# Performance work log

Measured on AMD Instinct MI355X. Metric: run time of the kernel, lower is better.

Reference implementation:

```python
import jax, jax.numpy as jnp
import numpy as np

N_NODES = 100000
N_EDGES = 1600000
IN_CH = 128
HID = 128
N_REL = 8


def setup_inputs() -> dict:
    key = jax.random.key(0)
    k_x, k_src, k_dst, k_et, k_w, k_root, k_b = jax.random.split(key, 7)
    x = jax.random.normal(k_x, (N_NODES, IN_CH), dtype=jnp.float32)
    src = jax.random.randint(k_src, (N_EDGES,), 0, N_NODES)
    dst = jax.random.randint(k_dst, (N_EDGES,), 0, N_NODES)
    edge_index = jnp.stack([src, dst], axis=0)  # [2, E]
    edge_type = jax.random.randint(k_et, (N_EDGES,), 0, N_REL)
    # RGCNConv parameters: per-relation weight, root (self-loop) weight, bias
    scale = 1.0 / np.sqrt(IN_CH)
    W = jax.random.normal(k_w, (N_REL, IN_CH, HID), dtype=jnp.float32) * scale
    root = jax.random.normal(k_root, (IN_CH, HID), dtype=jnp.float32) * scale
    bias = jnp.zeros((HID,), dtype=jnp.float32)
    return {"x": x, "edge_index": edge_index, "edge_type": edge_type,
            "W": W, "root": root, "bias": bias}


def reference(x, edge_index, edge_type, W, root, bias):
    # RGCNConv (mean aggregation per relation) + ReLU. Dropout is identity (eval mode).
    # Aggregate-then-transform: mathematically identical to PyG's
    # transform-then-aggregate since the relation transform is linear,
    # but far cheaper (R matmuls over N nodes instead of E edges).
    N = x.shape[0]
    n_rel = W.shape[0]
    src, dst = edge_index[0], edge_index[1]
    x_src = x[src]  # [E, C] gathered neighbor features
    out = x @ root + bias  # root / self-loop term
    for r in range(n_rel):
        mask = (edge_type == r)
        xm = jnp.where(mask[:, None], x_src, 0.0)  # zero out other relations
        agg = jax.ops.segment_sum(xm, dst, num_segments=N)  # [N, C]
        cnt = jax.ops.segment_sum(mask.astype(x.dtype), dst, num_segments=N)
        mean_agg = agg / jnp.maximum(cnt, 1.0)[:, None]
        out = out + mean_agg @ W[r]
    return jax.nn.relu(out)
```

## Files before the change

### kernel.cpp

```cpp
#include <hip/hip_runtime.h>

#define NREL 8
#define CH   128
#define YW   1152
#define YWD  (YW / 2)
#define NCB2 18

#define SCAN_ITEMS   16
#define SCAN_THREADS 256
#define SCAN_CHUNK   (SCAN_ITEMS * SCAN_THREADS)
#define SCAN_SHIFT   12

typedef short  short8v __attribute__((ext_vector_type(8)));
typedef float  f32x4   __attribute__((ext_vector_type(4)));

__device__ __forceinline__ unsigned short f2bf(float f) {
    union { float f; unsigned u; } v; v.f = f;
    return (unsigned short)((v.u + 0x7FFFu + ((v.u >> 16) & 1u)) >> 16);
}
__device__ __forceinline__ float lof(unsigned u) {
    union { unsigned u; float f; } v; v.u = u << 16; return v.f;
}
__device__ __forceinline__ float hif(unsigned u) {
    union { unsigned u; float f; } v; v.u = u & 0xFFFF0000u; return v.f;
}
__device__ __forceinline__ void gload_lds16(const void* g, void* l) {
    __builtin_amdgcn_global_load_lds(
        (const __attribute__((address_space(1))) unsigned int*)g,
        (__attribute__((address_space(3))) unsigned int*)l, 16, 0, 0);
}

__global__ __launch_bounds__(256) void bt2_kernel(
    const float* __restrict__ W, const float* __restrict__ root,
    unsigned short* __restrict__ Bt2)
{
    int idx = blockIdx.x * blockDim.x + threadIdx.x;
    if (idx >= YW * CH) return;
    int rc = idx >> 7, k = idx & 127;
    int r = rc >> 7, c = rc & 127;
    float v = (r < NREL) ? W[(size_t)(r * CH + k) * CH + c]
                         : root[(size_t)k * CH + c];
    Bt2[idx] = f2bf(v);
}

__global__ __launch_bounds__(256) void hist_rank_kernel(
    const int* __restrict__ dst, const int* __restrict__ et,
    int* __restrict__ hist, int* __restrict__ rank, int E)
{
    int e = blockIdx.x * blockDim.x + threadIdx.x;
    if (e < E) rank[e] = atomicAdd(&hist[dst[e] * NREL + et[e]], 1);
}

__global__ __launch_bounds__(SCAN_THREADS) void scan1_kernel(
    const int* __restrict__ hist, int* __restrict__ pad_offs,
    int* __restrict__ partials, int S)
{
    __shared__ int lds[SCAN_THREADS];
    int t = threadIdx.x;
    int base = blockIdx.x * SCAN_CHUNK + t * SCAN_ITEMS;
    int v[SCAN_ITEMS];
    int s = 0;
#pragma unroll
    for (int j = 0; j < SCAN_ITEMS; j++) {
        int idx = base + j;
        int h = (idx < S) ? hist[idx] : 0;
        v[j] = s; s += h;
    }
    int run = s;
    lds[t] = run; __syncthreads();
    for (int off = 1; off < SCAN_THREADS; off <<= 1) {
        int y = (t >= off) ? lds[t - off] : 0;
        __syncthreads();
        run += y; lds[t] = run; __syncthreads();
    }
    int tb = run - s;
    if (t == SCAN_THREADS - 1) partials[blockIdx.x] = run;
#pragma unroll
    for (int j = 0; j < SCAN_ITEMS; j++) {
        int idx = base + j;
        if (idx < S) pad_offs[idx] = tb + v[j];
    }
}

__global__ __launch_bounds__(SCAN_THREADS) void scan2_kernel(
    int* __restrict__ partials, int NB)
{
    __shared__ int lds[SCAN_THREADS];
    int t = threadIdx.x;
    int s = (t < NB) ? partials[t] : 0;
    int run = s;
    lds[t] = run; __syncthreads();
    for (int off = 1; off < SCAN_THREADS; off <<= 1) {
        int y = (t >= off) ? lds[t - off] : 0;
        __syncthreads();
        run += y; lds[t] = run; __syncthreads();
    }
    if (t < NB) partials[t] = run - s;
}

__global__ __launch_bounds__(256) void finalize_kernel(
    int* __restrict__ pad_offs, const int* __restrict__ partials, int S, int E)
{
    int i = blockIdx.x * blockDim.x + threadIdx.x;
    if (i < S)       pad_offs[i] += partials[i >> SCAN_SHIFT];
    else if (i == S) pad_offs[i] = E;
}

__global__ __launch_bounds__(512, 6) void ygemm_fill_kernel(
    const float* __restrict__ x,
    const unsigned short* __restrict__ Bt2,
    unsigned short* __restrict__ y,
    int N,
    const int* __restrict__ src, const int* __restrict__ dst,
    const int* __restrict__ et, const int* __restrict__ rank,
    const int* __restrict__ pad_offs,
    int* __restrict__ perm, int E, int epb)
{
    __shared__ __align__(16) unsigned short As[128 * 128];
    __shared__ __align__(16) unsigned short Bs[64 * 128];

    int tid  = threadIdx.x;
    int lane = tid & 63;
    int wid  = tid >> 6;
    int wm   = wid >> 2;
    int wn   = wid & 3;
    int r15  = lane & 15;
    int kg   = lane >> 4;
    int n0   = blockIdx.x * 128;

    int eb   = blockIdx.x * epb;
    int elim = eb + epb; if (elim > E) elim = E;
    int p0 = -1, p1 = -1, p2 = -1, p3 = -1;
    int v0 = 0, v1 = 0, v2 = 0, v3 = 0;
    {
        int e0 = eb + tid;
        int e1 = e0 + 512, e2 = e1 + 512, e3 = e2 + 512;
        if (e0 < elim) { int t0 = et[e0]; v0 = (src[e0] << 3) | t0;
                         p0 = pad_offs[dst[e0] * NREL + t0] + rank[e0]; }
        if (e1 < elim) { int t1 = et[e1]; v1 = (src[e1] << 3) | t1;
                         p1 = pad_offs[dst[e1] * NREL + t1] + rank[e1]; }
        if (e2 < elim) { int t2 = et[e2]; v2 = (src[e2] << 3) | t2;
                         p2 = pad_offs[dst[e2] * NREL + t2] + rank[e2]; }
        if (e3 < elim) { int t3 = et[e3]; v3 = (src[e3] << 3) | t3;
                         p3 = pad_offs[dst[e3] * NREL + t3] + rank[e3]; }
    }

    {
        int row = tid >> 2;
        int kq  = tid & 3;
        int gn  = n0 + row; if (gn >= N) gn = N - 1;
        const float* xp = x + (size_t)gn * CH + kq * 32;
#pragma unroll
        for (int s8 = 0; s8 < 4; ++s8) {
            float4 f0 = *(const float4*)(xp + s8 * 8);
            float4 f1 = *(const float4*)(xp + s8 * 8 + 4);
            uint4 v;
            v.x = f2bf(f0.x) | ((unsigned)f2bf(f0.y) << 16);
            v.y = f2bf(f0.z) | ((unsigned)f2bf(f0.w) << 16);
            v.z = f2bf(f1.x) | ((unsigned)f2bf(f1.y) << 16);
            v.w = f2bf(f1.z) | ((unsigned)f2bf(f1.w) << 16);
            int slot = kq * 4 + s8;
            int phys = slot ^ (row & 15);
            *(uint4*)&As[row * 128 + phys * 8] = v;
        }
    }

    for (int cb = 0; cb < NCB2; ++cb) {
#pragma unroll
        for (int i = 0; i < 2; ++i) {
            int chunk = wid * 2 + i;
            int col   = chunk * 4 + (lane >> 4);
            int slot  = (lane & 15) ^ (col & 15);
            const char* srcp = (const char*)(Bt2 + (size_t)(cb * 64 + col) * CH + slot * 8);
            gload_lds16(srcp, &Bs[chunk * 512]);
        }
        __syncthreads();

        if      (cb == 1) { if (p0 >= 0) perm[p0] = v0; }
        else if (cb == 2) { if (p1 >= 0) perm[p1] = v1; }
        else if (cb == 3) { if (p2 >= 0) perm[p2] = v2; }
        else if (cb == 4) { if (p3 >= 0) perm[p3] = v3; }

        f32x4 acc[4];
#pragma unroll
        for (int i = 0; i < 4; i++) acc[i] = f32x4{0.f, 0.f, 0.f, 0.f};

#pragma unroll
        for (int ks = 0; ks < 4; ++ks) {
            short8v a[4], b;
#pragma unroll
            for (int mr = 0; mr < 4; ++mr) {
                int row  = wm * 64 + mr * 16 + r15;
                int phys = (ks * 4 + kg) ^ (row & 15);
                a[mr] = *(const short8v*)&As[row * 128 + phys * 8];
            }
            {
                int col  = wn * 16 + r15;
                int phys = (ks * 4 + kg) ^ (col & 15);
                b = *(const short8v*)&Bs[col * 128 + phys * 8];
            }
#pragma unroll
            for (int mr = 0; mr < 4; ++mr)
                acc[mr] = __builtin_amdgcn_mfma_f32_16x16x32_bf16(
                    a[mr], b, acc[mr], 0, 0, 0);
        }

#pragma unroll
        for (int mr = 0; mr < 4; ++mr) {
#pragma unroll
            for (int reg = 0; reg < 4; ++reg) {
                int gr = n0 + wm * 64 + mr * 16 + kg * 4 + reg;
                if (gr >= N) continue;
                int gc = cb * 64 + wn * 16 + r15;
                y[(size_t)gr * YW + gc] = f2bf(acc[mr][reg]);
            }
        }
        __syncthreads();
    }
}

__global__ __launch_bounds__(256) void gather_kernel(
    const unsigned short* __restrict__ y,
    const int* __restrict__ perm,
    const int* __restrict__ pad_offs,
    const int* __restrict__ hist,
    const float* __restrict__ bias,
    float* __restrict__ out, int N)
{
    int wid  = threadIdx.x >> 6;
    int lane = threadIdx.x & 63;
    int n    = blockIdx.x * 4 + wid;
    if (n >= N) return;

    int beg = pad_offs[n * NREL];
    int end = pad_offs[n * NREL + NREL];

    int4 h0 = *(const int4*)(hist + (size_t)n * NREL);
    int4 h1 = *(const int4*)(hist + (size_t)n * NREL + 4);
    float iw0 = 1.0f / (float)max(h0.x, 1);
    float iw1 = 1.0f / (float)max(h0.y, 1);
    float iw2 = 1.0f / (float)max(h0.z, 1);
    float iw3 = 1.0f / (float)max(h0.w, 1);
    float iw4 = 1.0f / (float)max(h1.x, 1);
    float iw5 = 1.0f / (float)max(h1.y, 1);
    float iw6 = 1.0f / (float)max(h1.z, 1);
    float iw7 = 1.0f / (float)max(h1.w, 1);

    const unsigned* y32 = (const unsigned*)y;
    float a0 = 0.f, a1 = 0.f;

    for (int blk = beg; blk < end; blk += 64) {
        int m = end - blk; if (m > 64) m = 64;
        int   rv = 0;
        float wv = 0.f;
        if (lane < m) {
            int pv  = perm[blk + lane];
            int rel = pv & 7;
            rv = pv + (pv >> 3);
            float wa = (rel & 1) ? iw1 : iw0;
            float wb = (rel & 1) ? iw3 : iw2;
            float wc = (rel & 1) ? iw5 : iw4;
            float wd = (rel & 1) ? iw7 : iw6;
            float we_ = (rel & 2) ? wb : wa;
            float wf  = (rel & 2) ? wd : wc;
            wv = (rel & 4) ? wf : we_;
        }

        int j = 0;
#define EDGE_LOAD(K) \
            int   p##K = __shfl(rv, j + K);                     \
            float w##K = __shfl(wv, j + K);                     \
            unsigned u##K = y32[(size_t)p##K * 64 + lane];
#define EDGE_ACC(K) \
            a0 += w##K * lof(u##K); a1 += w##K * hif(u##K);

        for (; j + 16 <= m; j += 16) {
            EDGE_LOAD(0) EDGE_LOAD(1) EDGE_LOAD(2)  EDGE_LOAD(3)
            EDGE_LOAD(4) EDGE_LOAD(5) EDGE_LOAD(6)  EDGE_LOAD(7)
            EDGE_LOAD(8) EDGE_LOAD(9) EDGE_LOAD(10) EDGE_LOAD(11)
            EDGE_LOAD(12) EDGE_LOAD(13) EDGE_LOAD(14) EDGE_LOAD(15)
            EDGE_ACC(0)  EDGE_ACC(1)  EDGE_ACC(2)  EDGE_ACC(3)
            EDGE_ACC(4)  EDGE_ACC(5)  EDGE_ACC(6)  EDGE_ACC(7)
            EDGE_ACC(8)  EDGE_ACC(9)  EDGE_ACC(10) EDGE_ACC(11)
            EDGE_ACC(12) EDGE_ACC(13) EDGE_ACC(14) EDGE_ACC(15)
        }
        if (j + 8 <= m) {
            EDGE_LOAD(0) EDGE_LOAD(1) EDGE_LOAD(2) EDGE_LOAD(3)
            EDGE_LOAD(4) EDGE_LOAD(5) EDGE_LOAD(6) EDGE_LOAD(7)
            EDGE_ACC(0) EDGE_ACC(1) EDGE_ACC(2) EDGE_ACC(3)
            EDGE_ACC(4) EDGE_ACC(5) EDGE_ACC(6) EDGE_ACC(7)
            j += 8;
        }
        if (j + 4 <= m) {
            EDGE_LOAD(0) EDGE_LOAD(1) EDGE_LOAD(2) EDGE_LOAD(3)
            EDGE_ACC(0) EDGE_ACC(1) EDGE_ACC(2) EDGE_ACC(3)
            j += 4;
        }
        for (; j < m; ++j) {
            EDGE_LOAD(0)
            EDGE_ACC(0)
        }
#undef EDGE_LOAD
#undef EDGE_ACC
    }

    unsigned ur = y32[(size_t)n * YWD + (NREL * CH / 2) + lane];
    float o0 = a0 + lof(ur) + bias[lane * 2];
    float o1 = a1 + hif(ur) + bias[lane * 2 + 1];
    float2 ov;
    ov.x = fmaxf(o0, 0.f);
    ov.y = fmaxf(o1, 0.f);
    *(float2*)(out + (size_t)n * CH + lane * 2) = ov;
}

extern "C" void kernel_launch(void* const* d_in, const int* in_sizes, int n_in,
                              void* d_out, int out_size, void* d_ws, size_t ws_size,
                              hipStream_t stream)
{
    const float* x    = (const float*)d_in[0];
    const int*   ei   = (const int*)d_in[1];
    const int*   et   = (const int*)d_in[2];
    const float* W    = (const float*)d_in[3];
    const float* root = (const float*)d_in[4];
    const float* bias = (const float*)d_in[5];
    float*       out  = (float*)d_out;

    int N = in_sizes[0] / CH;
    int E = in_sizes[2];
    const int* src = ei;
    const int* dst = ei + E;

    int S  = N * NREL;
    int NB = (S + SCAN_CHUNK - 1) / SCAN_CHUNK;

    unsigned short* y   = (unsigned short*)d_ws;
    unsigned short* Bt2 = y + (size_t)N * YW;
    int* hist     = (int*)(Bt2 + (size_t)YW * CH);
    int* pad_offs = hist + S;
    int* partials = pad_offs + S + 1;
    int* perm     = partials + 256;
    int* rank     = perm + E;

    hipMemsetAsync(hist, 0, (size_t)S * sizeof(int), stream);

    int egrid = (E + 255) / 256;
    int G     = (N + 127) / 128;
    int epb   = ((E + G - 1) / G + 2047) & ~2047;

    bt2_kernel<<<(YW * CH + 255) / 256, 256, 0, stream>>>(W, root, Bt2);
    hist_rank_kernel<<<egrid, 256, 0, stream>>>(dst, et, hist, rank, E);
    scan1_kernel<<<NB, SCAN_THREADS, 0, stream>>>(hist, pad_offs, partials, S);
    scan2_kernel<<<1, SCAN_THREADS, 0, stream>>>(partials, NB);
    finalize_kernel<<<(S + 256) / 256, 256, 0, stream>>>(pad_offs, partials, S, E);
    ygemm_fill_kernel<<<G, 512, 0, stream>>>(x, Bt2, y, N,
                                             src, dst, et, rank, pad_offs,
                                             perm, E, epb);
    gather_kernel<<<(N + 3) / 4, 256, 0, stream>>>(y, perm, pad_offs, hist, bias, out, N);
}
```

Before: 282.5 us.

## Keep A fragments in registers and load B directly, dropping LDS staging

The fused GEMM+perm-fill kernel no longer stages the x tile or the Bt2 column blocks through shared memory. Each wave converts its A rows straight from global into register fragments once, and loads B fragments directly from global (L2-resident) per column block. This removes both __syncthreads per iteration and the LDS traffic. It costs more registers (launch bounds occupancy lowered from 6 to 4) and duplicate B loads across waves.

Measured after the change: 342.2 us. 1.21x slower.

```diff
diff --git a/kernel.cpp b/kernel.cpp
--- a/kernel.cpp
+++ b/kernel.cpp
@@ -23,11 +23,6 @@
 }
 __device__ __forceinline__ float hif(unsigned u) {
     union { unsigned u; float f; } v; v.u = u & 0xFFFF0000u; return v.f;
-}
-__device__ __forceinline__ void gload_lds16(const void* g, void* l) {
-    __builtin_amdgcn_global_load_lds(
-        (const __attribute__((address_space(1))) unsigned int*)g,
-        (__attribute__((address_space(3))) unsigned int*)l, 16, 0, 0);
 }
 
 __global__ __launch_bounds__(256) void bt2_kernel(
@@ -106,7 +101,7 @@
     else if (i == S) pad_offs[i] = E;
 }
 
-__global__ __launch_bounds__(512, 6) void ygemm_fill_kernel(
+__global__ __launch_bounds__(512, 4) void ygemm_fill_kernel(
     const float* __restrict__ x,
     const unsigned short* __restrict__ Bt2,
     unsigned short* __restrict__ y,
@@ -116,9 +111,6 @@
     const int* __restrict__ pad_offs,
     int* __restrict__ perm, int E, int epb)
 {
-    __shared__ __align__(16) unsigned short As[128 * 128];
-    __shared__ __align__(16) unsigned short Bs[64 * 128];
-
     int tid  = threadIdx.x;
     int lane = tid & 63;
     int wid  = tid >> 6;
@@ -145,36 +137,32 @@
                          p3 = pad_offs[dst[e3] * NREL + t3] + rank[e3]; }
     }
 
-    {
-        int row = tid >> 2;
-        int kq  = tid & 3;
-        int gn  = n0 + row; if (gn >= N) gn = N - 1;
-        const float* xp = x + (size_t)gn * CH + kq * 32;
-#pragma unroll
-        for (int s8 = 0; s8 < 4; ++s8) {
-            float4 f0 = *(const float4*)(xp + s8 * 8);
-            float4 f1 = *(const float4*)(xp + s8 * 8 + 4);
-            uint4 v;
-            v.x = f2bf(f0.x) | ((unsigned)f2bf(f0.y) << 16);
-            v.y = f2bf(f0.z) | ((unsigned)f2bf(f0.w) << 16);
-            v.z = f2bf(f1.x) | ((unsigned)f2bf(f1.y) << 16);
-            v.w = f2bf(f1.z) | ((unsigned)f2bf(f1.w) << 16);
-            int slot = kq * 4 + s8;
-            int phys = slot ^ (row & 15);
-            *(uint4*)&As[row * 128 + phys * 8] = v;
+    short8v a[4][4];
+#pragma unroll
+    for (int mr = 0; mr < 4; ++mr) {
+        int row = n0 + wm * 64 + mr * 16 + r15;
+        if (row >= N) row = N - 1;
+        const float* ap = x + (size_t)row * CH + kg * 8;
+#pragma unroll
+        for (int ks = 0; ks < 4; ++ks) {
+            float4 lo = *(const float4*)(ap + ks * 32);
+            float4 hi = *(const float4*)(ap + ks * 32 + 4);
+            union { short8v s; unsigned u[4]; } t;
+            t.u[0] = f2bf(lo.x) | ((unsigned)f2bf(lo.y) << 16);
+            t.u[1] = f2bf(lo.z) | ((unsigned)f2bf(lo.w) << 16);
+            t.u[2] = f2bf(hi.x) | ((unsigned)f2bf(hi.y) << 16);
+            t.u[3] = f2bf(hi.z) | ((unsigned)f2bf(hi.w) << 16);
+            a[mr][ks] = t.s;
         }
     }
 
     for (int cb = 0; cb < NCB2; ++cb) {
-#pragma unroll
-        for (int i = 0; i < 2; ++i) {
-            int chunk = wid * 2 + i;
-            int col   = chunk * 4 + (lane >> 4);
-            int slot  = (lane & 15) ^ (col & 15);
-            const char* srcp = (const char*)(Bt2 + (size_t)(cb * 64 + col) * CH + slot * 8);
-            gload_lds16(srcp, &Bs[chunk * 512]);
-        }
-        __syncthreads();
+        int col = cb * 64 + wn * 16 + r15;
+        const unsigned short* bp = Bt2 + (size_t)col * CH + kg * 8;
+        short8v b[4];
+#pragma unroll
+        for (int ks = 0; ks < 4; ++ks)
+            b[ks] = *(const short8v*)(bp + ks * 32);
 
         if      (cb == 1) { if (p0 >= 0) perm[p0] = v0; }
         else if (cb == 2) { if (p1 >= 0) perm[p1] = v1; }
@@ -186,36 +174,22 @@
         for (int i = 0; i < 4; i++) acc[i] = f32x4{0.f, 0.f, 0.f, 0.f};
 
 #pragma unroll
-        for (int ks = 0; ks < 4; ++ks) {
-            short8v a[4], b;
-#pragma unroll
-            for (int mr = 0; mr < 4; ++mr) {
-                int row  = wm * 64 + mr * 16 + r15;
-                int phys = (ks * 4 + kg) ^ (row & 15);
-                a[mr] = *(const short8v*)&As[row * 128 + phys * 8];
-            }
-            {
-                int col  = wn * 16 + r15;
-                int phys = (ks * 4 + kg) ^ (col & 15);
-                b = *(const short8v*)&Bs[col * 128 + phys * 8];
-            }
+        for (int ks = 0; ks < 4; ++ks)
 #pragma unroll
             for (int mr = 0; mr < 4; ++mr)
                 acc[mr] = __builtin_amdgcn_mfma_f32_16x16x32_bf16(
-                    a[mr], b, acc[mr], 0, 0, 0);
-        }
-
+                    a[mr][ks], b[ks], acc[mr], 0, 0, 0);
+
+        int gc = cb * 64 + wn * 16 + r15;
 #pragma unroll
         for (int mr = 0; mr < 4; ++mr) {
 #pragma unroll
             for (int reg = 0; reg < 4; ++reg) {
                 int gr = n0 + wm * 64 + mr * 16 + kg * 4 + reg;
                 if (gr >= N) continue;
-                int gc = cb * 64 + wn * 16 + r15;
                 y[(size_t)gr * YW + gc] = f2bf(acc[mr][reg]);
             }
         }
-        __syncthreads();
     }
 }
 
```
